# Optimization experiments

Hardware: AMD Instinct MI355X
Metric: run time of the kernel (lower is better)

## Reference

```python
import jax, jax.numpy as jnp
import numpy as np
from math import factorial

# ---------------- real Wigner-3j coefficients (l <= 2) ----------------

def _w3j_c(l1, l2, l3, m1, m2, m3):
    if m1 + m2 + m3 != 0:
        return 0.0
    f = factorial
    pref = ((-1.0) ** (l1 - l2 - m3)) * np.sqrt(
        f(l1 + l2 - l3) * f(l1 - l2 + l3) * f(-l1 + l2 + l3) / f(l1 + l2 + l3 + 1)
        * f(l1 + m1) * f(l1 - m1) * f(l2 + m2) * f(l2 - m2) * f(l3 + m3) * f(l3 - m3))
    s = 0.0
    for t in range(0, l1 + l2 - l3 + 1):
        ds = [t, l3 - l2 + t + m1, l3 - l1 + t - m2, l1 + l2 - l3 - t, l1 - t - m1, l2 - t + m2]
        if min(ds) < 0:
            continue
        den = 1
        for d in ds:
            den *= f(d)
        s += ((-1.0) ** t) / den
    return pref * s

def _u_real(l):
    # complex->real spherical-harmonic change of basis (rows: mu=-l..l, cols: m=-l..l)
    U = np.zeros((2 * l + 1, 2 * l + 1), dtype=np.complex128)
    U[l, l] = 1.0
    for m in range(1, l + 1):
        U[l + m, l + m] = ((-1) ** m) / np.sqrt(2)
        U[l + m, l - m] = 1.0 / np.sqrt(2)
        U[l - m, l - m] = 1j / np.sqrt(2)
        U[l - m, l + m] = -1j * ((-1) ** m) / np.sqrt(2)
    return U

def _real_w3j(l1, l2, l3):
    W = np.zeros((2 * l1 + 1, 2 * l2 + 1, 2 * l3 + 1), dtype=np.complex128)
    for a, m1 in enumerate(range(-l1, l1 + 1)):
        for b, m2 in enumerate(range(-l2, l2 + 1)):
            for c, m3 in enumerate(range(-l3, l3 + 1)):
                W[a, b, c] = _w3j_c(l1, l2, l3, m1, m2, m3)
    C = np.einsum('am,bn,co,mno->abc', _u_real(l1), _u_real(l2), _u_real(l3), W)
    C = C.real + C.imag  # each entry is purely real or purely imaginary
    n = np.linalg.norm(C)
    if n > 0:
        C = C / n
    return jnp.asarray(C, dtype=jnp.float32)

W3J = {(l1, l2, l3): _real_w3j(l1, l2, l3)
       for l1 in range(3) for l2 in range(3) for l3 in range(3)
       if abs(l1 - l2) <= l3 <= l1 + l2}

SH_OFF = [0, 1, 4]
RELU_GAIN = float(np.sqrt(2.0))  # normalize2mom gain for ReLU

# ---------------- building blocks ----------------

def tp_instructions(in_ls):
    # input irrep blocks have parity (-1)**l (0e,1o,2e); sh = 0e+1o+2e; out = 0e+1o+2e
    ins = []
    for i1, l1 in enumerate(in_ls):
        for l2 in range(3):
            for l3 in range(3):
                if abs(l1 - l2) <= l3 <= l1 + l2 and ((-1) ** (l1 + l2)) == (-1) ** l3:
                    ins.append((i1, l1, l2, l3))
    return ins

def sh_l2(d):
    # component-normalized real spherical harmonics of unit vectors, l=0..2
    x, y, z = d[:, 0], d[:, 1], d[:, 2]
    s3, s15, s5 = np.sqrt(3.0), np.sqrt(15.0), np.sqrt(5.0)
    sh0 = jnp.ones_like(x)[:, None]
    sh1 = jnp.stack([s3 * y, s3 * z, s3 * x], axis=1)
    sh2 = jnp.stack([s15 * x * y, s15 * y * z, (s5 / 2) * (3 * z * z - 1.0),
                     s15 * x * z, (s15 / 2) * (x * x - y * y)], axis=1)
    return jnp.concatenate([sh0, sh1, sh2], axis=1)

def radial_basis(d, num=11, start=0.0, end=8.0):
    values = jnp.linspace(start, end, num)
    step = values[1] - values[0]
    diff = (d[:, None] - values) / step
    return jnp.exp(-(diff * diff)) / 1.12  # e3nn soft_one_hot_linspace 'gaussian'

def radial_net(rb, w1, w2):
    h = jax.nn.relu(rb @ (w1 / np.sqrt(w1.shape[0]))) * RELU_GAIN
    return h @ (w2 / np.sqrt(w2.shape[0]))

def equiv_conv(pos, x, src, dst, rw1, rw2, in_ls, mul_in, C):
    E = src.shape[0]
    vec = pos[src] - pos[dst]                      # (E,3)
    dist = jnp.sqrt(jnp.sum(vec * vec, axis=1))    # (E,)
    w = radial_net(radial_basis(dist), rw1, rw2)   # (E, weight_numel)
    dirs = vec / jnp.maximum(dist, 1e-12)[:, None]
    sh = sh_l2(dirs)                               # (E,9)
    xd = x[dst]                                    # edge gather
    ins = tp_instructions(in_ls)
    fan = {0: 0, 1: 0, 2: 0}
    for (_, l1, l2, l3) in ins:
        fan[l3] += mul_in
    in_off = np.cumsum([0] + [mul_in * (2 * l + 1) for l in in_ls])
    out = [jnp.zeros((E, C, 2 * l3 + 1), x.dtype) for l3 in range(3)]
    woff = 0
    for (i1, l1, l2, l3) in ins:
        x1 = xd[:, in_off[i1]:in_off[i1 + 1]].reshape(E, mul_in, 2 * l1 + 1)
        shb = sh[:, SH_OFF[l2]:SH_OFF[l2] + 2 * l2 + 1]
        wi = w[:, woff:woff + mul_in * C].reshape(E, mul_in, C)
        woff += mul_in * C
        alpha = np.sqrt(2 * l3 + 1) / np.sqrt(fan[l3])
        out[l3] = out[l3] + alpha * jnp.einsum('eui,ej,euw,ijk->ewk', x1, shb, wi, W3J[(l1, l2, l3)])
    msg = jnp.concatenate([o.reshape(E, -1) for o in out], axis=1)
    return jax.ops.segment_sum(msg, src, num_segments=pos.shape[0])  # scatter_add onto src

def self_interaction(x, W, mul_in):
    # x: mul_in x (0e+1o+2e); W: (3, mul_in, mul_out)
    outs, off = [], 0
    for l in range(3):
        d = 2 * l + 1
        b = x[:, off:off + mul_in * d].reshape(-1, mul_in, d)
        off += mul_in * d
        outs.append((jnp.einsum('nui,uw->nwi', b, W[l]) / np.sqrt(mul_in)).reshape(x.shape[0], -1))
    return jnp.concatenate(outs, axis=1)

def pointwise_nonlin(x, b, mul):
    outs, off = [], 0
    for l in range(3):
        d = 2 * l + 1
        blk = x[:, off:off + mul * d]
        off += mul * d
        if l == 0:
            outs.append(jax.nn.softplus(blk + b[0]))
        else:
            v = blk.reshape(-1, mul, d)
            gate = jax.nn.softplus(jnp.sqrt(jnp.sum(v * v, axis=2) + 1e-24) + b[l])
            outs.append((v * gate[:, :, None]).reshape(x.shape[0], -1))
    return jnp.concatenate(outs, axis=1)

def pointwise_norm(x):
    return x / (jnp.linalg.norm(x, axis=1, keepdims=True) + 1e-6)

def backbone(pos, features, edge_index, si0_w, c1_rw1, c1_rw2, si1_w, nl1_b,
             c2_rw1, c2_rw2, si2_w, nl2_b, c3_rw1, c3_rw2, si3_w, nl3_b, fsi_w):
    src, dst = edge_index[0], edge_index[1]
    x = features @ si0_w / np.sqrt(features.shape[1])          # 64x0e -> 128x0e
    x = equiv_conv(pos, x, src, dst, c1_rw1, c1_rw2, [0], 128, 128)
    x = pointwise_norm(x)
    x = self_interaction(x, si1_w, 128)
    x = pointwise_nonlin(x, nl1_b, 128)
    x = equiv_conv(pos, x, src, dst, c2_rw1, c2_rw2, [0, 1, 2], 128, 64)
    x = pointwise_norm(x)
    x = self_interaction(x, si2_w, 64)
    x = pointwise_nonlin(x, nl2_b, 64)
    x = equiv_conv(pos, x, src, dst, c3_rw1, c3_rw2, [0, 1, 2], 64, 32)
    x = pointwise_norm(x)
    x = self_interaction(x, si3_w, 32)
    x = pointwise_nonlin(x, nl3_b, 32)
    x = self_interaction(x, fsi_w, 32)
    return x[:, :32]  # scalar (0e) part

# ---------------- harness ----------------

N_NODES, N_EDGES, FEAT = 512, 2048, 64

def setup_inputs() -> dict:
    key = jax.random.key(0)
    ks = jax.random.split(key, 20)
    src = jax.random.randint(ks[0], (N_EDGES,), 0, N_NODES)
    # avoid self-loops (zero-length edges are degenerate for normalize/grad)
    dst = (src + 1 + jax.random.randint(ks[1], (N_EDGES,), 0, N_NODES - 1)) % N_NODES
    edge_index = jnp.stack([src, dst]).astype(jnp.int64)
    rn = lambda k, s: jax.random.normal(k, s, dtype=jnp.float32)
    return {
        'pos': rn(ks[2], (N_NODES, 3)),
        'features': rn(ks[3], (N_NODES, FEAT)),
        'edge_index': edge_index,
        'si0_w': rn(ks[4], (FEAT, 128)),
        'c1_rw1': rn(ks[5], (11, 12)), 'c1_rw2': rn(ks[6], (12, 3 * 128 * 128)),
        'si1_w': rn(ks[7], (3, 128, 128)), 'nl1_b': jnp.zeros((3,), jnp.float32),
        'c2_rw1': rn(ks[8], (11, 12)), 'c2_rw2': rn(ks[9], (12, 11 * 128 * 64)),
        'si2_w': rn(ks[10], (3, 64, 64)), 'nl2_b': jnp.zeros((3,), jnp.float32),
        'c3_rw1': rn(ks[11], (11, 12)), 'c3_rw2': rn(ks[12], (12, 11 * 64 * 32)),
        'si3_w': rn(ks[13], (3, 32, 32)), 'nl3_b': jnp.zeros((3,), jnp.float32),
        'fsi_w': rn(ks[14], (3, 32, 32)),
    }

def reference(pos, features, edge_index, si0_w, c1_rw1, c1_rw2, si1_w, nl1_b,
              c2_rw1, c2_rw2, si2_w, nl2_b, c3_rw1, c3_rw2, si3_w, nl3_b, fsi_w):
    return backbone(pos, features, edge_index, si0_w, c1_rw1, c1_rw2, si1_w, nl1_b,
                    c2_rw1, c2_rw2, si2_w, nl2_b, c3_rw1, c3_rw2, si3_w, nl3_b, fsi_w)
```

## Files before the change

### kernel.cpp

```cpp
#include <hip/hip_runtime.h>
#include <cmath>
#include <cstdint>

#define NNODES 512
#define NEDGES 2048

typedef _Float16 half2v __attribute__((ext_vector_type(2)));

#define OFF_W3J   0
#define OFF_SH    512
#define OFF_H1    (OFF_SH + NEDGES*9)
#define OFF_H2    (OFF_H1 + NEDGES*6)
#define OFF_H3    (OFF_H2 + NEDGES*6)
#define OFF_W2P1  (OFF_H3 + NEDGES*6)
#define OFF_W2P2  (OFF_W2P1 + 6*49152)
#define OFF_W2P3  (OFF_W2P2 + 6*90112)
#define OFF_XH    (OFF_W2P3 + 6*22528)
#define OFF_XB    (OFF_XH + NNODES*576)
#define OFF_MSGA  (OFF_XB + NNODES*1152)
#define OFF_CNT   (OFF_MSGA + NEDGES*576)
#define OFF_COFF  (OFF_CNT + 512)
#define OFF_LIST  (OFF_COFF + 1024)
#define OFF_RANK  (OFF_LIST + 2048)
#define OFF_MSGB  (OFF_RANK + 2048)
#define WS_NEED_SPLIT ((size_t)(OFF_MSGB + NEDGES*576) * 4)

__device__ __forceinline__ unsigned int packh2f(float a, float b){
  half2v h; h.x=(_Float16)a; h.y=(_Float16)b;
  return __builtin_bit_cast(unsigned int, h);
}
__device__ __forceinline__ half2v u2h2(unsigned int u){ return __builtin_bit_cast(half2v, u); }
__device__ __forceinline__ float dot2f(unsigned int a, unsigned int b, float c){
#if __has_builtin(__builtin_amdgcn_fdot2)
  return __builtin_amdgcn_fdot2(u2h2(a), u2h2(b), c, false);
#else
  half2v ha=u2h2(a), hb=u2h2(b);
  return c + (float)ha.x*(float)hb.x + (float)ha.y*(float)hb.y;
#endif
}
__device__ __forceinline__ unsigned int pk2(float a, float b){
#if __has_builtin(__builtin_amdgcn_cvt_pkrtz)
  auto h=__builtin_amdgcn_cvt_pkrtz(a,b);
  return __builtin_bit_cast(unsigned int,h);
#else
  return packh2f(a,b);
#endif
}
__device__ __forceinline__ unsigned short f2h(float f){
  _Float16 h=(_Float16)f; return __builtin_bit_cast(unsigned short,h);
}
__device__ __forceinline__ float softplusf(float v){ return fmaxf(v,0.f)+log1pf(expf(-fabsf(v))); }

__device__ double dfact(int n){ double f=1.0; for(int i=2;i<=n;++i) f*=(double)i; return f; }

__device__ double w3j_c_dev(int l1,int l2,int l3,int m1,int m2,int m3){
  if (m1+m2+m3 != 0) return 0.0;
  int p = l1 - l2 - m3;
  double sign = (((p%2)+2)%2) ? -1.0 : 1.0;
  double pref = sign*sqrt(dfact(l1+l2-l3)*dfact(l1-l2+l3)*dfact(-l1+l2+l3)/dfact(l1+l2+l3+1)
              *dfact(l1+m1)*dfact(l1-m1)*dfact(l2+m2)*dfact(l2-m2)*dfact(l3+m3)*dfact(l3-m3));
  double s=0.0;
  for (int t=0;t<=l1+l2-l3;++t){
    int d0=t, d1v=l3-l2+t+m1, d2v=l3-l1+t-m2, d3v=l1+l2-l3-t, d4=l1-t-m1, d5=l2-t+m2;
    if (d0<0||d1v<0||d2v<0||d3v<0||d4<0||d5<0) continue;
    double den=dfact(d0)*dfact(d1v)*dfact(d2v)*dfact(d3v)*dfact(d4)*dfact(d5);
    s += ((t&1)?-1.0:1.0)/den;
  }
  return pref*s;
}

__device__ void u_real_dev(int l, double Ur[5][5], double Ui[5][5]){
  for(int a=0;a<5;++a)for(int b=0;b<5;++b){Ur[a][b]=0.0;Ui[a][b]=0.0;}
  Ur[l][l]=1.0;
  double inv2 = 1.0/sqrt(2.0);
  for(int m=1;m<=l;++m){
    double sgn = (m&1)?-1.0:1.0;
    Ur[l+m][l+m] = sgn*inv2;
    Ur[l+m][l-m] = inv2;
    Ui[l-m][l-m] = inv2;
    Ui[l-m][l+m] = -sgn*inv2;
  }
}

__global__ void w3j_kernel(float* __restrict__ out){
  const int L1[11]={0,0,0,1,1,1,1,2,2,2,2};
  const int L2[11]={0,1,2,0,1,1,2,0,1,2,2};
  const int L3[11]={0,1,2,1,0,2,1,2,1,0,2};
  const int OFF[11]={0,1,10,35,44,53,98,143,168,213,238};
  int t = blockIdx.x;
  int tid = threadIdx.x;
  int l1=L1[t], l2=L2[t], l3=L3[t];
  int d1=2*l1+1, d2=2*l2+1, d3=2*l3+1;
  int sz=d1*d2*d3;
  __shared__ double Wt[125];
  __shared__ double U1r[5][5],U1i[5][5],U2r[5][5],U2i[5][5],U3r[5][5],U3i[5][5];
  __shared__ double Cv[125];
  __shared__ double red[128];
  for(int idx=tid; idx<sz; idx+=128){
    int a=idx/(d2*d3), rem=idx%(d2*d3), b=rem/d3, c=rem%d3;
    Wt[idx]=w3j_c_dev(l1,l2,l3,a-l1,b-l2,c-l3);
  }
  if(tid==0) u_real_dev(l1,U1r,U1i);
  if(tid==1) u_real_dev(l2,U2r,U2i);
  if(tid==2) u_real_dev(l3,U3r,U3i);
  __syncthreads();
  for(int idx=tid; idx<sz; idx+=128){
    int a=idx/(d2*d3), rem=idx%(d2*d3), b=rem/d3, c=rem%d3;
    double cr=0.0, ci=0.0;
    for(int m=0;m<d1;++m)for(int n=0;n<d2;++n){
      double t2r = U1r[a][m]*U2r[b][n]-U1i[a][m]*U2i[b][n];
      double t2i = U1r[a][m]*U2i[b][n]+U1i[a][m]*U2r[b][n];
      if (t2r==0.0 && t2i==0.0) continue;
      for(int o=0;o<d3;++o){
        double wv=Wt[(m*d2+n)*d3+o];
        if (wv==0.0) continue;
        double t3r=t2r*U3r[c][o]-t2i*U3i[c][o];
        double t3i=t2r*U3i[c][o]+t2i*U3r[c][o];
        cr += t3r*wv; ci += t3i*wv;
      }
    }
    Cv[idx]=cr+ci;
  }
  __syncthreads();
  double s=0.0;
  for(int idx=tid; idx<sz; idx+=128) s+=Cv[idx]*Cv[idx];
  red[tid]=s; __syncthreads();
  for(int d=64; d>0; d>>=1){ if(tid<d) red[tid]+=red[tid+d]; __syncthreads(); }
  double nrm = sqrt(red[0]);
  double inv = (nrm>0.0)?1.0/nrm:0.0;
  for(int idx=tid; idx<sz; idx+=128) out[OFF[t]+idx]=(float)(Cv[idx]*inv);
}

__global__ void edge_prep_kernel(const float* __restrict__ pos, const int* __restrict__ ei,
    const float* __restrict__ rw1a, const float* __restrict__ rw1b, const float* __restrict__ rw1c,
    float* __restrict__ sh, unsigned int* __restrict__ h1, unsigned int* __restrict__ h2,
    unsigned int* __restrict__ h3){
  int e = blockIdx.x*blockDim.x+threadIdx.x;
  if (e>=NEDGES) return;
  int s = ei[e], d = ei[NEDGES+e];
  float vx=pos[3*s]-pos[3*d], vy=pos[3*s+1]-pos[3*d+1], vz=pos[3*s+2]-pos[3*d+2];
  float dist=sqrtf(vx*vx+vy*vy+vz*vz);
  float dm = fmaxf(dist,1e-12f);
  float x=vx/dm, y=vy/dm, z=vz/dm;
  const float s3=sqrtf(3.f), s15=sqrtf(15.f), s5=sqrtf(5.f);
  float shv[9];
  shv[0]=1.f; shv[1]=s3*y; shv[2]=s3*z; shv[3]=s3*x;
  shv[4]=s15*x*y; shv[5]=s15*y*z; shv[6]=0.5f*s5*(3.f*z*z-1.f); shv[7]=s15*x*z; shv[8]=0.5f*s15*(x*x-y*y);
  #pragma unroll
  for(int i=0;i<9;++i) sh[e*9+i]=shv[i];
  float rb[11];
  #pragma unroll
  for(int i=0;i<11;++i){ float diff=(dist-0.8f*(float)i)*(1.f/0.8f); rb[i]=expf(-diff*diff)*(1.f/1.12f); }
  const float c1 = 1.f/sqrtf(11.f);
  const float c2 = sqrtf(2.f)/sqrtf(12.f);
  const float* rws[3]={rw1a,rw1b,rw1c};
  unsigned int* outs[3]={h1,h2,h3};
  for(int L=0;L<3;++L){
    float hv[12];
    #pragma unroll
    for(int r=0;r<12;++r){
      float t=0.f;
      #pragma unroll
      for(int k=0;k<11;++k) t+=rb[k]*rws[L][k*12+r];
      t*=c1;
      hv[r]=fmaxf(t,0.f)*c2;
    }
    #pragma unroll
    for(int r2=0;r2<6;++r2) outs[L][e*6+r2]=packh2f(hv[2*r2],hv[2*r2+1]);
  }
}

__global__ void w2pack_kernel(const float* __restrict__ w2, unsigned int* __restrict__ out, int nW){
  int idx=blockIdx.x*256+threadIdx.x;
  if(idx>=6*nW) return;
  int r2=idx/nW, c=idx-r2*nW;
  out[idx]=packh2f(w2[(size_t)(2*r2)*nW+c], w2[(size_t)(2*r2+1)*nW+c]);
}

__global__ __launch_bounds__(256) void csr_rank_kernel(const int* __restrict__ src,
    int* __restrict__ cnt, int* __restrict__ rankA){
  __shared__ int s_src[NEDGES];
  int tid=threadIdx.x;
  int4* s4=(int4*)s_src;
  const int4* g4=(const int4*)src;
  for(int i=tid;i<NEDGES/4;i+=256) s4[i]=g4[i];
  __syncthreads();
  int e=blockIdx.x*256+tid;
  int s=s_src[e];
  int lt=0, tot=0;
  for(int b=0;b<NEDGES/4;b+=8){
    int4 v[8];
    #pragma unroll
    for(int k=0;k<8;++k) v[k]=s4[b+k];
    #pragma unroll
    for(int k=0;k<8;++k){
      int j0=4*(b+k);
      tot += ((v[k].x==s)?1:0)+((v[k].y==s)?1:0)+((v[k].z==s)?1:0)+((v[k].w==s)?1:0);
      lt  += ((v[k].x==s&&j0<e)?1:0)+((v[k].y==s&&j0+1<e)?1:0)+((v[k].z==s&&j0+2<e)?1:0)+((v[k].w==s&&j0+3<e)?1:0);
    }
  }
  rankA[e]=lt;
  if(lt==tot-1) cnt[s]=tot;
}

__global__ void csr_scan_kernel(const int* __restrict__ cnt, int* __restrict__ coff){
  __shared__ int s[NNODES];
  int tid=threadIdx.x;
  s[tid]=cnt[tid];
  __syncthreads();
  for(int d=1;d<NNODES;d<<=1){
    int v=(tid>=d)?s[tid-d]:0;
    __syncthreads();
    s[tid]+=v;
    __syncthreads();
  }
  coff[tid+1]=s[tid];
  if(tid==0) coff[0]=0;
}

__global__ void csr_scatter_kernel(const int* __restrict__ src, const int* __restrict__ coff,
    const int* __restrict__ rankA, int* __restrict__ list){
  int e=blockIdx.x*256+threadIdx.x;
  int s=src[e];
  list[coff[s]+rankA[e]]=e;
}

__global__ void si0_kernel(const float* __restrict__ feat, const float* __restrict__ w,
                           unsigned int* __restrict__ xh){
  __shared__ float s_f[64];
  __shared__ unsigned short s_v[128];
  int n=blockIdx.x, tid=threadIdx.x;
  if(tid<64) s_f[tid]=feat[n*64+tid];
  __syncthreads();
  float acc=0.f;
  for(int u=0;u<64;++u) acc += s_f[u]*w[u*128+tid];
  s_v[tid]=f2h(acc*0.125f);
  __syncthreads();
  if(tid<64) xh[(size_t)n*64+tid]=((unsigned int)s_v[2*tid+1]<<16)|s_v[2*tid];
}

struct CInstr { int l1,l2,l3,woff,w3off; float alpha; };
struct LayerArg { CInstr ins[3][4]; int cnt[3]; int gOf[8]; int rank[8]; int nxg[3]; };

template<int MUL,int C,int EB,int NL,int USPLIT,int D3,int L1v>
__device__ __forceinline__ void instr_body(
  const unsigned int* __restrict__ W2h, int nW, int woff,
  const unsigned int (&hreg)[EB][6],
  const uint4* s_xp4, const float* sB,
  float (&acc)[EB][D3], int ubase, int uOff2, int w)
{
  constexpr int D1=2*L1v+1;
  constexpr int MULZ=MUL/USPLIT;
  constexpr int MZ2=MULZ/2;
  constexpr int UC=256/C;
  constexpr int CHZ=MUL/(UC*USPLIT);
  constexpr int CB=(L1v==0)?0:((L1v==1)?MZ2:4*MZ2);
  static_assert(EB==4,"EB must be 4");
  static_assert(CHZ>=2 && (CHZ&1)==0,"CHZ even");
  const unsigned int* Wp = W2h + (size_t)woff + (size_t)ubase*C + w;
  float a2[EB][D1];
  #pragma unroll
  for(int e=0;e<EB;++e){
    #pragma unroll
    for(int i=0;i<D1;++i) a2[e][i]=0.f;
  }
  #pragma unroll 2
  for(int u2=0;u2<CHZ/2;++u2){
    unsigned int wv0[6],wv1[6];
    #pragma unroll
    for(int r=0;r<6;++r){
      wv0[r]=Wp[(size_t)r*nW + (size_t)(2*u2)*C];
      wv1[r]=Wp[(size_t)r*nW + (size_t)(2*u2+1)*C];
    }
    unsigned int wi2[EB];
    #pragma unroll
    for(int e=0;e<EB;++e){
      float w0=0.f,w1=0.f;
      #pragma unroll
      for(int r=0;r<6;++r){ w0=dot2f(hreg[e][r],wv0[r],w0); w1=dot2f(hreg[e][r],wv1[r],w1); }
      wi2[e]=pk2(w0,w1);
    }
    #pragma unroll
    for(int i=0;i<D1;++i){
      uint4 xv = s_xp4[CB + i*MZ2 + uOff2 + u2];
      a2[0][i]=dot2f(wi2[0],xv.x,a2[0][i]);
      a2[1][i]=dot2f(wi2[1],xv.y,a2[1][i]);
      a2[2][i]=dot2f(wi2[2],xv.z,a2[2][i]);
      a2[3][i]=dot2f(wi2[3],xv.w,a2[3][i]);
    }
  }
  #pragma unroll
  for(int e=0;e<EB;++e){
    #pragma unroll
    for(int k=0;k<D3;++k){
      float s=0.f;
      #pragma unroll
      for(int i=0;i<D1;++i) s += a2[e][i]*sB[e*25+i*5+k];
      acc[e][k]+=s;
    }
  }
}

template<int MUL,int C,int EB,int NL,int USPLIT,int D3,int NINS>
__device__ __forceinline__ void conv_main(
  const unsigned int* __restrict__ W2h, int nW,
  const unsigned int (&hreg)[EB][6],
  const uint4* s_xp4, const float* s_B, float* s_red, unsigned short* s_msg,
  unsigned int* __restrict__ msg, const LayerArg& la, int g, int e0,
  int w, int uc, int ubase, int uOff2)
{
  constexpr int UC=256/C;
  const int tid=threadIdx.x;
  float acc[EB][D3];
  #pragma unroll
  for(int e=0;e<EB;++e){
    #pragma unroll
    for(int k=0;k<D3;++k) acc[e][k]=0.f;
  }
  #pragma unroll
  for(int ii=0;ii<NINS;++ii){
    const int l1v=la.ins[g][ii].l1;
    const int woff=la.ins[g][ii].woff;
    switch(l1v){
      case 0: instr_body<MUL,C,EB,NL,USPLIT,D3,0>(W2h,nW,woff,hreg,s_xp4,s_B+ii*EB*25,acc,ubase,uOff2,w); break;
      case 1: instr_body<MUL,C,EB,NL,USPLIT,D3,1>(W2h,nW,woff,hreg,s_xp4,s_B+ii*EB*25,acc,ubase,uOff2,w); break;
      default: instr_body<MUL,C,EB,NL,USPLIT,D3,2>(W2h,nW,woff,hreg,s_xp4,s_B+ii*EB*25,acc,ubase,uOff2,w); break;
    }
  }
  constexpr int L3v=(D3-1)/2;
  constexpr int base32=(L3v==0)?0:((L3v==1)?C/2:2*C);
  constexpr int seg32=C*D3/2;
  for(int e=0;e<EB;++e){
    #pragma unroll
    for(int k=0;k<D3;++k) s_red[k*256+tid]=acc[e][k];
    __syncthreads();
    if(uc==0){
      #pragma unroll
      for(int k=0;k<D3;++k){
        float s=0.f;
        #pragma unroll
        for(int c2=0;c2<UC;++c2) s+=s_red[k*256+c2*C+w];
        s_msg[(e*C+w)*D3+k]=f2h(s);
      }
    }
    __syncthreads();
  }
  const unsigned int* sm32=(const unsigned int*)s_msg;
  for(int ix=tid; ix<EB*seg32; ix+=256){
    int e=ix/seg32, o=ix-e*seg32;
    msg[(size_t)(e0+e)*(9*C/2) + base32 + o] = sm32[e*seg32+o];
  }
}

template<int MUL,int C,int EB,int NL,int USPLIT>
__global__ __launch_bounds__(256,4) void conv_kernel(
  const unsigned int* __restrict__ xh, const unsigned int* __restrict__ W2h, int nW,
  const unsigned int* __restrict__ hb, const float* __restrict__ shb,
  const int* __restrict__ dstp, const float* __restrict__ w3j,
  unsigned int* __restrict__ msg0, unsigned int* __restrict__ msg1, LayerArg la)
{
  constexpr int MUL2=MUL/2;
  constexpr int MULZ=MUL/USPLIT;
  constexpr int MZ2=MULZ/2;
  constexpr int ROW=(NL==1)?MUL2:9*MUL2;
  constexpr int SROW=(NL==1)?MZ2:9*MZ2;
  constexpr int UC=256/C;
  constexpr int CHZ=MUL/(UC*USPLIT);
  constexpr int NB=NEDGES/EB;
  __shared__ unsigned int s_xp[SROW*EB];
  __shared__ float s_B[4*EB*25];
  __shared__ float s_red[5*256];
  __shared__ unsigned short s_msg[EB*C*5];
  int tid=threadIdx.x;
  int bid=blockIdx.x;
  int xcd=bid&7, slot=bid>>3;
  int g=la.gOf[xcd];
  int idx=slot*la.nxg[g]+la.rank[xcd];
  if(idx>=NB*USPLIT) return;
  int zz=idx/NB, et=idx-zz*NB;
  int e0=et*EB;
  unsigned int* msg=(zz==0)?msg0:msg1;
  for(int ix=tid; ix<EB*SROW; ix+=256){
    int e=ix/SROW, c=ix-(ix/SROW)*SROW;
    int l1,i,u2l;
    if(NL==1){ l1=0;i=0;u2l=c; }
    else{
      if(c<MZ2){l1=0;i=0;u2l=c;}
      else if(c<4*MZ2){int t=c-MZ2;i=t/MZ2;u2l=t-i*MZ2;l1=1;}
      else{int t=c-4*MZ2;i=t/MZ2;u2l=t-i*MZ2;l1=2;}
    }
    int gb=(l1==0)?0:((l1==1)?MUL2:4*MUL2);
    int dn=dstp[e0+e];
    s_xp[c*EB+e]=xh[(size_t)dn*ROW + gb + i*MUL2 + zz*MZ2 + u2l];
  }
  int nIns=la.cnt[g];
  for(int ix=tid; ix<nIns*EB*25; ix+=256){
    int ii=ix/(EB*25); int rem=ix%(EB*25); int e=rem/25; int q=rem%25;
    int i=q/5,k=q%5;
    CInstr I=la.ins[g][ii];
    int d1=2*I.l1+1,d2=2*I.l2+1,d3v=2*I.l3+1;
    float v=0.f;
    if(i<d1&&k<d3v){
      int sho=I.l2*I.l2;
      for(int j=0;j<d2;++j) v+=shb[(size_t)(e0+e)*9+sho+j]*w3j[I.w3off+(i*d2+j)*d3v+k];
      v*=I.alpha;
    }
    s_B[(ii*EB+e)*25+q]=v;
  }
  __syncthreads();
  int w=tid%C, uc=tid/C;
  int ubase=zz*MULZ+uc*CHZ;
  int uOff2=uc*(CHZ/2);
  unsigned int hreg[EB][6];
  #pragma unroll
  for(int e=0;e<EB;++e){
    #pragma unroll
    for(int r=0;r<6;++r) hreg[e][r]=hb[(size_t)(e0+e)*6+r];
  }
  const uint4* s_xp4=(const uint4*)s_xp;
  if(NL==1){
    if(g==0)      conv_main<MUL,C,EB,NL,USPLIT,1,1>(W2h,nW,hreg,s_xp4,s_B,s_red,s_msg,msg,la,g,e0,w,uc,ubase,uOff2);
    else if(g==1) conv_main<MUL,C,EB,NL,USPLIT,3,1>(W2h,nW,hreg,s_xp4,s_B,s_red,s_msg,msg,la,g,e0,w,uc,ubase,uOff2);
    else          conv_main<MUL,C,EB,NL,USPLIT,5,1>(W2h,nW,hreg,s_xp4,s_B,s_red,s_msg,msg,la,g,e0,w,uc,ubase,uOff2);
  }else{
    if(g==0)      conv_main<MUL,C,EB,NL,USPLIT,1,3>(W2h,nW,hreg,s_xp4,s_B,s_red,s_msg,msg,la,g,e0,w,uc,ubase,uOff2);
    else if(g==1) conv_main<MUL,C,EB,NL,USPLIT,3,4>(W2h,nW,hreg,s_xp4,s_B,s_red,s_msg,msg,la,g,e0,w,uc,ubase,uOff2);
    else          conv_main<MUL,C,EB,NL,USPLIT,5,4>(W2h,nW,hreg,s_xp4,s_B,s_red,s_msg,msg,la,g,e0,w,uc,ubase,uOff2);
  }
}

__global__ void aggregate_kernel(const unsigned int* __restrict__ msg0,
                                 const unsigned int* __restrict__ msg1,
                                 const int* __restrict__ coff, const int* __restrict__ list,
                                 float* __restrict__ xout, int W32){
  int n=blockIdx.x;
  int b=coff[n], en=coff[n+1];
  for(int c32=threadIdx.x;c32<W32;c32+=blockDim.x){
    float a0=0.f,a1=0.f;
    for(int j=b;j<en;++j){
      size_t o=(size_t)list[j]*W32+c32;
      half2v p=u2h2(msg0[o]); a0+=(float)p.x; a1+=(float)p.y;
      if(msg1){ half2v q=u2h2(msg1[o]); a0+=(float)q.x; a1+=(float)q.y; }
    }
    xout[(size_t)n*(2*W32)+2*c32]=a0;
    xout[(size_t)n*(2*W32)+2*c32+1]=a1;
  }
}

template<int MUL>
__global__ void post_kernel(const float* __restrict__ xin, const float* __restrict__ siw,
                            const float* __restrict__ nlb, unsigned int* __restrict__ xh){
  constexpr int ROW=9*MUL/2;
  __shared__ float s_in[MUL*9];
  __shared__ unsigned short s_out[MUL*9];
  __shared__ float red[256];
  int n=blockIdx.x, tid=threadIdx.x;
  float ss=0.f;
  for(int c=tid;c<MUL*9;c+=256){ float v=xin[(size_t)n*MUL*9+c]; s_in[c]=v; ss+=v*v; }
  red[tid]=ss; __syncthreads();
  for(int d=128;d>0;d>>=1){ if(tid<d) red[tid]+=red[tid+d]; __syncthreads(); }
  float scale=1.f/(sqrtf(red[0])+1e-6f);
  const float inv=scale/sqrtf((float)MUL);
  float b0=nlb[0], b1=nlb[1], b2=nlb[2];
  for(int p=tid;p<3*MUL;p+=256){
    int l=p/MUL, wo=p%MUL;
    if(l==0){
      const float* Wl=siw;
      float a=0.f;
      for(int u=0;u<MUL;++u) a+=s_in[u]*Wl[(size_t)u*MUL+wo];
      s_out[wo]=f2h(softplusf(a*inv+b0));
    } else if(l==1){
      const float* Wl=siw+(size_t)MUL*MUL;
      float v0=0.f,v1=0.f,v2=0.f;
      for(int u=0;u<MUL;++u){
        float wv=Wl[(size_t)u*MUL+wo];
        int bi=MUL+u*3;
        v0+=s_in[bi]*wv; v1+=s_in[bi+1]*wv; v2+=s_in[bi+2]*wv;
      }
      v0*=inv; v1*=inv; v2*=inv;
      float gate=softplusf(sqrtf(v0*v0+v1*v1+v2*v2+1e-24f)+b1);
      int ob=MUL+wo*3;
      s_out[ob]=f2h(v0*gate); s_out[ob+1]=f2h(v1*gate); s_out[ob+2]=f2h(v2*gate);
    } else {
      const float* Wl=siw+(size_t)2*MUL*MUL;
      float v0=0.f,v1=0.f,v2=0.f,v3=0.f,v4=0.f;
      for(int u=0;u<MUL;++u){
        float wv=Wl[(size_t)u*MUL+wo];
        int bi=4*MUL+u*5;
        v0+=s_in[bi]*wv; v1+=s_in[bi+1]*wv; v2+=s_in[bi+2]*wv; v3+=s_in[bi+3]*wv; v4+=s_in[bi+4]*wv;
      }
      v0*=inv; v1*=inv; v2*=inv; v3*=inv; v4*=inv;
      float gate=softplusf(sqrtf(v0*v0+v1*v1+v2*v2+v3*v3+v4*v4+1e-24f)+b2);
      int ob=4*MUL+wo*5;
      s_out[ob]=f2h(v0*gate); s_out[ob+1]=f2h(v1*gate); s_out[ob+2]=f2h(v2*gate);
      s_out[ob+3]=f2h(v3*gate); s_out[ob+4]=f2h(v4*gate);
    }
  }
  __syncthreads();
  for(int p=tid;p<ROW;p+=256){
    int l,i,u2;
    if(p<MUL/2){l=0;i=0;u2=p;}
    else if(p<2*MUL){int t=p-MUL/2;i=t/(MUL/2);u2=t%(MUL/2);l=1;}
    else{int t=p-2*MUL;i=t/(MUL/2);u2=t%(MUL/2);l=2;}
    int d=2*l+1, sb=MUL*l*l;
    unsigned short a=s_out[sb+(2*u2)*d+i], bb=s_out[sb+(2*u2+1)*d+i];
    xh[(size_t)n*ROW+p]=((unsigned int)bb<<16)|a;
  }
}

__global__ void final_kernel(const unsigned int* __restrict__ xh, const float* __restrict__ fsi,
                             float* __restrict__ out){
  int gid=blockIdx.x*blockDim.x+threadIdx.x;
  if(gid>=NNODES*32) return;
  int n=gid/32, wo=gid%32;
  float s=0.f;
  for(int u2=0;u2<16;++u2){
    half2v p=u2h2(xh[(size_t)n*144+u2]);
    s += (float)p.x*fsi[(2*u2)*32+wo] + (float)p.y*fsi[(2*u2+1)*32+wo];
  }
  out[gid]=s*(1.f/sqrtf(32.f));
}

static int w3off_of(int l1,int l2,int l3){
  const int L1[11]={0,0,0,1,1,1,1,2,2,2,2};
  const int L2[11]={0,1,2,0,1,1,2,0,1,2,2};
  const int L3[11]={0,1,2,1,0,2,1,2,1,0,2};
  const int OFF[11]={0,1,10,35,44,53,98,143,168,213,238};
  for(int i=0;i<11;++i) if(L1[i]==l1&&L2[i]==l2&&L3[i]==l3) return OFF[i];
  return 0;
}

static void fill_map(LayerArg& la, const int alloc[3]){
  int x=0;
  for(int g=0;g<3;++g){
    la.nxg[g]=alloc[g];
    for(int r=0;r<alloc[g];++r){ la.gOf[x]=g; la.rank[x]=r; ++x; }
  }
}
static int gridS(const int alloc[3], int NBZ){
  int S=0;
  for(int g=0;g<3;++g){ int s=(NBZ+alloc[g]-1)/alloc[g]; if(s>S)S=s; }
  return S;
}

extern "C" void kernel_launch(void* const* d_in, const int* in_sizes, int n_in,
                              void* d_out, int out_size, void* d_ws, size_t ws_size,
                              hipStream_t stream) {
  const float* pos    = (const float*)d_in[0];
  const float* feat   = (const float*)d_in[1];
  const int*   ei     = (const int*)d_in[2];
  const float* si0w   = (const float*)d_in[3];
  const float* c1_rw1 = (const float*)d_in[4];
  const float* c1_rw2 = (const float*)d_in[5];
  const float* si1w   = (const float*)d_in[6];
  const float* nl1b   = (const float*)d_in[7];
  const float* c2_rw1 = (const float*)d_in[8];
  const float* c2_rw2 = (const float*)d_in[9];
  const float* si2w   = (const float*)d_in[10];
  const float* nl2b   = (const float*)d_in[11];
  const float* c3_rw1 = (const float*)d_in[12];
  const float* c3_rw2 = (const float*)d_in[13];
  const float* si3w   = (const float*)d_in[14];
  const float* nl3b   = (const float*)d_in[15];
  const float* fsiw   = (const float*)d_in[16];

  float* ws_f=(float*)d_ws;
  float* w3   = ws_f+OFF_W3J;
  float* sh   = ws_f+OFF_SH;
  unsigned int* h1   = (unsigned int*)(ws_f+OFF_H1);
  unsigned int* h2   = (unsigned int*)(ws_f+OFF_H2);
  unsigned int* h3   = (unsigned int*)(ws_f+OFF_H3);
  unsigned int* w2p1 = (unsigned int*)(ws_f+OFF_W2P1);
  unsigned int* w2p2 = (unsigned int*)(ws_f+OFF_W2P2);
  unsigned int* w2p3 = (unsigned int*)(ws_f+OFF_W2P3);
  unsigned int* xh   = (unsigned int*)(ws_f+OFF_XH);
  float* xb   = ws_f+OFF_XB;
  unsigned int* msgA = (unsigned int*)(ws_f+OFF_MSGA);
  unsigned int* msgB = (unsigned int*)(ws_f+OFF_MSGB);
  int* cnt    = (int*)(ws_f+OFF_CNT);
  int* coff   = (int*)(ws_f+OFF_COFF);
  int* clist  = (int*)(ws_f+OFF_LIST);
  int* rankA  = (int*)(ws_f+OFF_RANK);
  const int* src  = ei;
  const int* dstp = ei+NEDGES;

  const bool split = ws_size >= WS_NEED_SPLIT;
  const int NB = NEDGES/4;

  LayerArg la1{}, la2{}, la3{};
  {
    int step=128*128;
    for(int i=0;i<3;++i){
      CInstr I{0,i,i, i*step, w3off_of(0,i,i), (float)std::sqrt((2.0*i+1.0)/128.0)};
      la1.ins[i][la1.cnt[i]++]=I;
    }
  }
  const int insL[11][3]={{0,0,0},{0,1,1},{0,2,2},{1,0,1},{1,1,0},{1,1,2},{1,2,1},{2,0,2},{2,1,1},{2,2,0},{2,2,2}};
  auto build=[&](LayerArg& la, int mul, int Cc){
    int step=mul*Cc;
    int fan[3]={0,0,0};
    for(int i=0;i<11;++i) fan[insL[i][2]] += mul;
    for(int i=0;i<11;++i){
      int l1v=insL[i][0],l2v=insL[i][1],l3v=insL[i][2];
      CInstr I{l1v,l2v,l3v, i*step, w3off_of(l1v,l2v,l3v), (float)std::sqrt((2.0*l3v+1.0)/(double)fan[l3v])};
      la.ins[l3v][la.cnt[l3v]++]=I;
    }
  };
  build(la2,128,64);
  build(la3,64,32);

  const int alloc1[3]={3,3,2};
  const int alloc23[3]={2,3,3};
  fill_map(la1,alloc1);
  fill_map(la2,alloc23);
  fill_map(la3,alloc23);

  w3j_kernel<<<dim3(11),dim3(128),0,stream>>>(w3);
  edge_prep_kernel<<<dim3(NEDGES/256),dim3(256),0,stream>>>(pos,ei,c1_rw1,c2_rw1,c3_rw1, sh,h1,h2,h3);
  w2pack_kernel<<<dim3((6*49152+255)/256),dim3(256),0,stream>>>(c1_rw2,w2p1,49152);
  w2pack_kernel<<<dim3((6*90112+255)/256),dim3(256),0,stream>>>(c2_rw2,w2p2,90112);
  w2pack_kernel<<<dim3((6*22528+255)/256),dim3(256),0,stream>>>(c3_rw2,w2p3,22528);

  hipMemsetAsync(cnt,0,NNODES*sizeof(int),stream);
  csr_rank_kernel<<<dim3(NEDGES/256),dim3(256),0,stream>>>(src,cnt,rankA);
  csr_scan_kernel<<<dim3(1),dim3(NNODES),0,stream>>>(cnt,coff);
  csr_scatter_kernel<<<dim3(NEDGES/256),dim3(256),0,stream>>>(src,coff,rankA,clist);

  si0_kernel<<<dim3(NNODES),dim3(128),0,stream>>>(feat,si0w,xh);

  if(split){
    int S1=gridS(alloc1,NB*2), S23=gridS(alloc23,NB*2);
    conv_kernel<128,128,4,1,2><<<dim3(8*S1),dim3(256),0,stream>>>(xh,w2p1,3*128*128,h1,sh,dstp,w3,msgA,msgB,la1);
    aggregate_kernel<<<dim3(NNODES),dim3(256),0,stream>>>(msgA,msgB,coff,clist,xb,576);
    post_kernel<128><<<dim3(NNODES),dim3(256),0,stream>>>(xb,si1w,nl1b,xh);
    conv_kernel<128,64,4,3,2><<<dim3(8*S23),dim3(256),0,stream>>>(xh,w2p2,11*128*64,h2,sh,dstp,w3,msgA,msgB,la2);
    aggregate_kernel<<<dim3(NNODES),dim3(256),0,stream>>>(msgA,msgB,coff,clist,xb,288);
    post_kernel<64><<<dim3(NNODES),dim3(256),0,stream>>>(xb,si2w,nl2b,xh);
    conv_kernel<64,32,4,3,2><<<dim3(8*S23),dim3(256),0,stream>>>(xh,w2p3,11*64*32,h3,sh,dstp,w3,msgA,msgB,la3);
    aggregate_kernel<<<dim3(NNODES),dim3(256),0,stream>>>(msgA,msgB,coff,clist,xb,144);
    post_kernel<32><<<dim3(NNODES),dim3(256),0,stream>>>(xb,si3w,nl3b,xh);
  } else {
    int S1=gridS(alloc1,NB), S23=gridS(alloc23,NB);
    conv_kernel<128,128,4,1,1><<<dim3(8*S1),dim3(256),0,stream>>>(xh,w2p1,3*128*128,h1,sh,dstp,w3,msgA,msgA,la1);
    aggregate_kernel<<<dim3(NNODES),dim3(256),0,stream>>>(msgA,(const unsigned int*)nullptr,coff,clist,xb,576);
    post_kernel<128><<<dim3(NNODES),dim3(256),0,stream>>>(xb,si1w,nl1b,xh);
    conv_kernel<128,64,4,3,1><<<dim3(8*S23),dim3(256),0,stream>>>(xh,w2p2,11*128*64,h2,sh,dstp,w3,msgA,msgA,la2);
    aggregate_kernel<<<dim3(NNODES),dim3(256),0,stream>>>(msgA,(const unsigned int*)nullptr,coff,clist,xb,288);
    post_kernel<64><<<dim3(NNODES),dim3(256),0,stream>>>(xb,si2w,nl2b,xh);
    conv_kernel<64,32,4,3,1><<<dim3(8*S23),dim3(256),0,stream>>>(xh,w2p3,11*64*32,h3,sh,dstp,w3,msgA,msgA,la3);
    aggregate_kernel<<<dim3(NNODES),dim3(256),0,stream>>>(msgA,(const unsigned int*)nullptr,coff,clist,xb,144);
    post_kernel<32><<<dim3(NNODES),dim3(256),0,stream>>>(xb,si3w,nl3b,xh);
  }

  final_kernel<<<dim3((NNODES*32+255)/256),dim3(256),0,stream>>>(xh,fsiw,(float*)d_out);
}
```

Before: 342.4 us.

## Precompute per-node weight products for layer-1 conv and split edge stage

For layer 1, whose instructions only pair l1 with l2=0 paths, the per-edge weight contraction is refactored into a per-node GEMM (V = x · W over radial basis index) computed once per node instead of once per edge. A light edge kernel then dots the radial features with the gathered V and multiplies by the spherical-harmonic/3j factor. This removes redundant per-edge GEMM work, since there are 4x more edges than nodes. It requires a new weight packing layout and reuses msgB as V storage, so layer 3 drops its split-K variant in favour of a single message buffer.

```diff
diff --git a/kernel.cpp b/kernel.cpp
--- a/kernel.cpp
+++ b/kernel.cpp
@@ -175,6 +175,82 @@
   if(idx>=6*nW) return;
   int r2=idx/nW, c=idx-r2*nW;
   out[idx]=packh2f(w2[(size_t)(2*r2)*nW+c], w2[(size_t)(2*r2+1)*nW+c]);
+}
+
+__global__ void w1pack_kernel(const float* __restrict__ w2, unsigned int* __restrict__ out){
+  int idx=blockIdx.x*256+threadIdx.x;
+  if(idx>=384*768) return;
+  int col=idx/768, rem=idx-col*768;
+  int r=rem/64, u2=rem-r*64;
+  int i=col>>7, w=col&127;
+  size_t s0=(size_t)r*49152 + i*16384 + (2*u2)*128 + w;
+  out[idx]=packh2f(w2[s0], w2[s0+128]);
+}
+
+__global__ __launch_bounds__(384) void vgemm1_kernel(const unsigned int* __restrict__ xh,
+    const unsigned int* __restrict__ w1p, unsigned int* __restrict__ V){
+  __shared__ __align__(16) unsigned int s_x[4][64];
+  int tid=threadIdx.x;
+  int n0=blockIdx.x*4;
+  for(int ix=tid; ix<256; ix+=384){ int n=ix>>6, u2=ix&63; s_x[n][u2]=xh[(size_t)(n0+n)*64+u2]; }
+  __syncthreads();
+  int col=tid;
+  float acc[4][12];
+  #pragma unroll
+  for(int n=0;n<4;++n)
+    #pragma unroll
+    for(int r=0;r<12;++r) acc[n][r]=0.f;
+  const uint4* Wp=(const uint4*)(w1p + (size_t)col*768);
+  for(int u4=0;u4<16;++u4){
+    uint4 xv[4];
+    #pragma unroll
+    for(int n=0;n<4;++n) xv[n]=((const uint4*)s_x[n])[u4];
+    #pragma unroll
+    for(int r=0;r<12;++r){
+      uint4 wv=Wp[r*16+u4];
+      #pragma unroll
+      for(int n=0;n<4;++n){
+        acc[n][r]=dot2f(xv[n].x,wv.x,acc[n][r]);
+        acc[n][r]=dot2f(xv[n].y,wv.y,acc[n][r]);
+        acc[n][r]=dot2f(xv[n].z,wv.z,acc[n][r]);
+        acc[n][r]=dot2f(xv[n].w,wv.w,acc[n][r]);
+      }
+    }
+  }
+  #pragma unroll
+  for(int n=0;n<4;++n)
+    #pragma unroll
+    for(int r2=0;r2<6;++r2)
+      V[((size_t)(n0+n)*384+col)*6+r2]=pk2(acc[n][2*r2],acc[n][2*r2+1]);
+}
+
+__global__ __launch_bounds__(384) void conv1_edge_kernel(const unsigned int* __restrict__ V,
+    const unsigned int* __restrict__ h1, const float* __restrict__ shb,
+    const int* __restrict__ dstp, const float* __restrict__ w3j,
+    unsigned int* __restrict__ msgA){
+  const int W3O[3]={0,1,10};
+  unsigned short* m16=(unsigned short*)msgA;
+  int tid=threadIdx.x;
+  int col=tid;
+  int i=col>>7, w=col&127;
+  int d3=2*i+1;
+  float alpha=sqrtf((float)(2*i+1))*(1.f/sqrtf(128.f));
+  int e0=blockIdx.x*2;
+  #pragma unroll
+  for(int s=0;s<2;++s){
+    int e=e0+s;
+    int n=dstp[e];
+    const unsigned int* vp=V+((size_t)n*384+col)*6;
+    float G=0.f;
+    #pragma unroll
+    for(int r2=0;r2<6;++r2) G=dot2f(h1[(size_t)e*6+r2], vp[r2], G);
+    int base=(i==0)?0:((i==1)?128:512);
+    for(int k=0;k<d3;++k){
+      float B=0.f;
+      for(int j=0;j<d3;++j) B += shb[(size_t)e*9+i*i+j]*w3j[W3O[i]+j*d3+k];
+      m16[(size_t)e*1152 + base + w*d3 + k]=f2h(G*B*alpha);
+    }
+  }
 }
 
 __global__ __launch_bounds__(256) void csr_rank_kernel(const int* __restrict__ src,
@@ -577,6 +653,7 @@
   float* xb   = ws_f+OFF_XB;
   unsigned int* msgA = (unsigned int*)(ws_f+OFF_MSGA);
   unsigned int* msgB = (unsigned int*)(ws_f+OFF_MSGB);
+  unsigned int* V    = msgB;
   int* cnt    = (int*)(ws_f+OFF_CNT);
   int* coff   = (int*)(ws_f+OFF_COFF);
   int* clist  = (int*)(ws_f+OFF_LIST);
@@ -617,7 +694,11 @@
 
   w3j_kernel<<<dim3(11),dim3(128),0,stream>>>(w3);
   edge_prep_kernel<<<dim3(NEDGES/256),dim3(256),0,stream>>>(pos,ei,c1_rw1,c2_rw1,c3_rw1, sh,h1,h2,h3);
-  w2pack_kernel<<<dim3((6*49152+255)/256),dim3(256),0,stream>>>(c1_rw2,w2p1,49152);
+  if(split){
+    w1pack_kernel<<<dim3((384*768+255)/256),dim3(256),0,stream>>>(c1_rw2,w2p1);
+  } else {
+    w2pack_kernel<<<dim3((6*49152+255)/256),dim3(256),0,stream>>>(c1_rw2,w2p1,49152);
+  }
   w2pack_kernel<<<dim3((6*90112+255)/256),dim3(256),0,stream>>>(c2_rw2,w2p2,90112);
   w2pack_kernel<<<dim3((6*22528+255)/256),dim3(256),0,stream>>>(c3_rw2,w2p3,22528);
 
@@ -629,15 +710,17 @@
   si0_kernel<<<dim3(NNODES),dim3(128),0,stream>>>(feat,si0w,xh);
 
   if(split){
-    int S1=gridS(alloc1,NB*2), S23=gridS(alloc23,NB*2);
-    conv_kernel<128,128,4,1,2><<<dim3(8*S1),dim3(256),0,stream>>>(xh,w2p1,3*128*128,h1,sh,dstp,w3,msgA,msgB,la1);
-    aggregate_kernel<<<dim3(NNODES),dim3(256),0,stream>>>(msgA,msgB,coff,clist,xb,576);
+    vgemm1_kernel<<<dim3(NNODES/4),dim3(384),0,stream>>>(xh,w2p1,V);
+    conv1_edge_kernel<<<dim3(NEDGES/2),dim3(384),0,stream>>>(V,h1,sh,dstp,w3,msgA);
+    aggregate_kernel<<<dim3(NNODES),dim3(256),0,stream>>>(msgA,(const unsigned int*)nullptr,coff,clist,xb,576);
     post_kernel<128><<<dim3(NNODES),dim3(256),0,stream>>>(xb,si1w,nl1b,xh);
+    int S23=gridS(alloc23,NB*2);
     conv_kernel<128,64,4,3,2><<<dim3(8*S23),dim3(256),0,stream>>>(xh,w2p2,11*128*64,h2,sh,dstp,w3,msgA,msgB,la2);
     aggregate_kernel<<<dim3(NNODES),dim3(256),0,stream>>>(msgA,msgB,coff,clist,xb,288);
     post_kernel<64><<<dim3(NNODES),dim3(256),0,stream>>>(xb,si2w,nl2b,xh);
-    conv_kernel<64,32,4,3,2><<<dim3(8*S23),dim3(256),0,stream>>>(xh,w2p3,11*64*32,h3,sh,dstp,w3,msgA,msgB,la3);
-    aggregate_kernel<<<dim3(NNODES),dim3(256),0,stream>>>(msgA,msgB,coff,clist,xb,144);
+    int S3=gridS(alloc23,NB);
+    conv_kernel<64,32,4,3,1><<<dim3(8*S3),dim3(256),0,stream>>>(xh,w2p3,11*64*32,h3,sh,dstp,w3,msgA,msgA,la3);
+    aggregate_kernel<<<dim3(NNODES),dim3(256),0,stream>>>(msgA,(const unsigned int*)nullptr,coff,clist,xb,144);
     post_kernel<32><<<dim3(NNODES),dim3(256),0,stream>>>(xb,si3w,nl3b,xh);
   } else {
     int S1=gridS(alloc1,NB), S23=gridS(alloc23,NB);
```

Result: no change. 335.7 us (-2.0%).
